# Optimization experiments

Hardware: AMD Instinct MI355X
Metric: run time of the kernel (lower is better)

The kernel has to match this reference:

```python
import jax, jax.numpy as jnp
import numpy as np
from jax import lax

H, W, C = 24, 8, 128
HW = H * W
PART = 4
SA_K = 49  # CBAM spatial-attention kernel size (default of CBAMBlock)
EPS = 1e-5


def conv2d(x, w, b, pad_h, pad_w):
    y = lax.conv_general_dilated(x, w, (1, 1), [(pad_h, pad_h), (pad_w, pad_w)],
                                 dimension_numbers=('NCHW', 'OIHW', 'NCHW'))
    return y + b[None, :, None, None]


def cbam(x, se_w1, se_w2, sa_w, sa_b):
    # Channel attention: shared MLP on global max- and avg-pooled descriptors.
    mx = x.max(axis=(2, 3))          # [n, c]
    av = x.mean(axis=(2, 3))         # [n, c]
    def se(v):
        return jax.nn.relu(v @ se_w1.T) @ se_w2.T
    ca = jax.nn.sigmoid(se(mx) + se(av))[:, :, None, None]
    out = x * ca
    # Spatial attention: 49x49 conv on [max, mean] over channels.
    smx = out.max(axis=1, keepdims=True)
    sav = out.mean(axis=1, keepdims=True)
    s = jnp.concatenate([smx, sav], axis=1)      # [n, 2, H, W]
    sa = jax.nn.sigmoid(conv2d(s, sa_w, sa_b, SA_K // 2, SA_K // 2))
    return out * sa + x


def position_aware_max(score6, dim):
    # score6: [p, g, hr, wr, hs, ws]; fixed-length (part_rows) row window,
    # start clamped to [0, h - part_rows] -> vectorized sliding-window max.
    part_rows = H // PART
    half = part_rows // 2
    starts = jnp.clip(jnp.arange(H) - half, 0, H - part_rows)
    if dim == 0:
        m = score6.max(axis=3)            # max over wr -> [p, g, hr, hs, ws]
        mi = jnp.moveaxis(m, 3, 0)        # [hs, p, g, hr, ws]
        def f(m_i, st):
            return lax.dynamic_slice_in_dim(m_i, st, part_rows, axis=2).max(axis=2)
        out = jax.vmap(f)(mi, starts)     # [h, p, g, ws]
    else:
        m = score6.max(axis=5)            # max over ws -> [p, g, hr, wr, hs]
        mi = jnp.moveaxis(m, 2, 0)        # [hr, p, g, wr, hs]
        def f(m_i, st):
            return lax.dynamic_slice_in_dim(m_i, st, part_rows, axis=3).max(axis=3)
        out = jax.vmap(f)(mi, starts)     # [h, p, g, wr]
    p, g = score6.shape[0], score6.shape[1]
    return jnp.moveaxis(out, 0, 2).reshape(p, g, HW)


def bn_eval(x, gamma, beta, mean, var):
    return (x - mean) * (gamma / jnp.sqrt(var + EPS)) + beta


def setup_inputs() -> dict:
    key = jax.random.key(0)
    ks = jax.random.split(key, 8)
    red = 16
    return {
        'prob_fea': jax.random.normal(ks[0], (32, C, H, W), jnp.float32),
        'gal_fea': jax.random.normal(ks[1], (32, C, H, W), jnp.float32),
        'se_w1': jax.random.normal(ks[2], (C // red, C), jnp.float32) * 0.05,
        'se_w2': jax.random.normal(ks[3], (C, C // red), jnp.float32) * 0.05,
        'sa_w': jax.random.normal(ks[4], (1, 2, SA_K, SA_K), jnp.float32) * 0.02,
        'sa_b': jnp.zeros((1,), jnp.float32),
        'bn_g': jnp.ones((1,), jnp.float32),
        'bn_b': jnp.zeros((1,), jnp.float32),
        'bn_m': jnp.zeros((1,), jnp.float32),
        'bn_v': jnp.ones((1,), jnp.float32),
        'fc_w': jnp.full((1, HW), 1.0 / HW, jnp.float32),
        'fc_b': jax.random.normal(ks[5], (1,), jnp.float32) * 0.01,
        'lbn_g': jnp.ones((1,), jnp.float32),
        'lbn_b': jnp.zeros((1,), jnp.float32),
        'lbn_m': jnp.zeros((1,), jnp.float32),
        'lbn_v': jnp.ones((1,), jnp.float32),
    }


def reference(prob_fea, gal_fea, se_w1, se_w2, sa_w, sa_b,
              bn_g, bn_b, bn_m, bn_v, fc_w, fc_b,
              lbn_g, lbn_b, lbn_m, lbn_v):
    pf = cbam(prob_fea, se_w1, se_w2, sa_w, sa_b)
    gf = cbam(gal_fea, se_w1, se_w2, sa_w, sa_b)
    p, g = pf.shape[0], gf.shape[0]
    pf = pf.reshape(p, C, HW)
    gf = gf.reshape(g, C, HW)
    # pairwise feature matching: [p, g, r(gal spatial), s(prob spatial)]
    score = jnp.einsum('pcs,gcr->pgrs', pf, gf)
    score6 = score.reshape(p, g, H, W, H, W)
    s1 = position_aware_max(score6, 0)  # [p, g, HW]
    s2 = position_aware_max(score6, 1)  # [p, g, HW]
    sc = jnp.concatenate([s1, s2], axis=-1).reshape(-1, HW)  # [p*g*2, HW]
    sc = bn_eval(sc, bn_g, bn_b, bn_m, bn_v)
    y = sc @ fc_w.T + fc_b                  # [p*g*2, 1]
    y = y.reshape(-1, 2).sum(axis=1, keepdims=True)
    y = bn_eval(y, lbn_g, lbn_b, lbn_m, lbn_v)
    return jax.nn.sigmoid(y).reshape(p, g)
```

## Files before the change

kernel.cpp:

```cpp
#include <hip/hip_runtime.h>
#include <hip/hip_bf16.h>

#define HH 24
#define WW 8
#define HWSZ 192
#define CC 128
#define EPSV 1e-5f

typedef __attribute__((ext_vector_type(8))) short bf16x8;
typedef __attribute__((ext_vector_type(4))) float f32x4;

__device__ __forceinline__ float sigmoidf_(float x) { return 1.0f / (1.0f + expf(-x)); }

__device__ __forceinline__ unsigned short f2bf(float f) {
    unsigned int u = __float_as_uint(f);
    unsigned int r = (u + 0x7fffu + ((u >> 16) & 1u)) >> 16;
    return (unsigned short)r;
}

__global__ __launch_bounds__(256) void cbam_kernel(
    const float* __restrict__ prob, const float* __restrict__ gal,
    const float* __restrict__ se_w1, const float* __restrict__ se_w2,
    const float* __restrict__ sa_w, const float* __restrict__ sa_b,
    __hip_bfloat16* __restrict__ pf_t, __hip_bfloat16* __restrict__ gf_t)
{
    __shared__ float mxs[CC], avs[CC], hid[16], cas[CC];
    __shared__ float smx[HWSZ], sav[HWSZ], sas[HWSZ];
    __shared__ float wbuf[2 * 49 * 49];

    int n = blockIdx.x;
    const float* x = (n < 32) ? prob + (size_t)n * CC * HWSZ : gal + (size_t)(n - 32) * CC * HWSZ;
    __hip_bfloat16* dst = (n < 32) ? pf_t + (size_t)n * HWSZ * CC : gf_t + (size_t)(n - 32) * HWSZ * CC;

    int tid = threadIdx.x, l = tid & 63, w = tid >> 6;

    for (int i = tid; i < 2 * 49 * 49; i += 256) wbuf[i] = sa_w[i];

    for (int c = w * 32; c < w * 32 + 32; ++c) {
        const float* row = x + c * HWSZ;
        float a = row[l], b = row[l + 64], d = row[l + 128];
        float mv = fmaxf(a, fmaxf(b, d));
        float sv = a + b + d;
        #pragma unroll
        for (int m = 1; m < 64; m <<= 1) {
            mv = fmaxf(mv, __shfl_xor(mv, m));
            sv += __shfl_xor(sv, m);
        }
        if (l == 0) { mxs[c] = mv; avs[c] = sv * (1.0f / HWSZ); }
    }
    __syncthreads();

    if (tid < 16) {
        int j = tid & 7;
        const float* v = (tid < 8) ? mxs : avs;
        float acc = 0.f;
        for (int c = 0; c < CC; ++c) acc += v[c] * se_w1[j * CC + c];
        hid[tid] = fmaxf(acc, 0.f);
    }
    __syncthreads();

    if (tid < CC) {
        float acc = 0.f;
        #pragma unroll
        for (int j = 0; j < 8; ++j) acc += (hid[j] + hid[8 + j]) * se_w2[tid * 8 + j];
        cas[tid] = sigmoidf_(acc);
    }
    __syncthreads();

    if (tid < HWSZ) {
        float mv = -INFINITY, sv = 0.f;
        for (int c = 0; c < CC; ++c) {
            float v = x[c * HWSZ + tid] * cas[c];
            mv = fmaxf(mv, v); sv += v;
        }
        smx[tid] = mv; sav[tid] = sv * (1.0f / CC);
    }
    __syncthreads();

    if (tid < HWSZ) {
        int y = tid >> 3, xx = tid & 7;
        float acc = sa_b[0];
        for (int iy = 0; iy < HH; ++iy) {
            int wy = iy - y + 24;
            const float* w0 = wbuf + wy * 49;
            const float* w1 = wbuf + 2401 + wy * 49;
            #pragma unroll
            for (int ix = 0; ix < WW; ++ix) {
                int wx = ix - xx + 24;
                float s0 = smx[iy * 8 + ix], s1 = sav[iy * 8 + ix];
                acc += s0 * w0[wx] + s1 * w1[wx];
            }
        }
        sas[tid] = sigmoidf_(acc);
    }
    __syncthreads();

    if (tid < HWSZ) {
        int s = tid;
        float sv = sas[s];
        unsigned int* dst32 = (unsigned int*)(dst + s * CC);
        for (int c = 0; c < CC; c += 2) {
            float v0 = x[c * HWSZ + s] * (1.f + cas[c] * sv);
            float v1 = x[(c + 1) * HWSZ + s] * (1.f + cas[c + 1] * sv);
            unsigned int pk = ((unsigned int)f2bf(v1) << 16) | (unsigned int)f2bf(v0);
            dst32[c >> 1] = pk;
        }
    }
}

__global__ __launch_bounds__(256) void score_kernel(
    const __hip_bfloat16* __restrict__ pf_t, const __hip_bfloat16* __restrict__ gf_t,
    const float* __restrict__ bn_g, const float* __restrict__ bn_b,
    const float* __restrict__ bn_m, const float* __restrict__ bn_v,
    const float* __restrict__ fc_w, const float* __restrict__ fc_b,
    const float* __restrict__ lbn_g, const float* __restrict__ lbn_b,
    const float* __restrict__ lbn_m, const float* __restrict__ lbn_v,
    float* __restrict__ out)
{
    __shared__ float M1[24 * HWSZ];
    __shared__ float M2[HWSZ * 24];
    __shared__ float red[8];

    int bi = blockIdx.x;
    int p = bi >> 5, g = bi & 31;
    int tid = threadIdx.x, l = tid & 63, w = tid >> 6;

    const __hip_bfloat16* A = gf_t + (size_t)g * HWSZ * CC;
    const __hip_bfloat16* B = pf_t + (size_t)p * HWSZ * CC;

    int row_a = l & 15;
    int koff = (l >> 4) * 8;

    bf16x8 afr[3][4];
    #pragma unroll
    for (int rt = 0; rt < 3; ++rt) {
        const __hip_bfloat16* ap = A + (w * 48 + rt * 16 + row_a) * CC + koff;
        #pragma unroll
        for (int ks = 0; ks < 4; ++ks)
            afr[rt][ks] = *(const bf16x8*)(ap + ks * 32);
    }

    for (int st = 0; st < 12; ++st) {
        bf16x8 bfr[4];
        const __hip_bfloat16* bp = B + (st * 16 + row_a) * CC + koff;
        #pragma unroll
        for (int ks = 0; ks < 4; ++ks) bfr[ks] = *(const bf16x8*)(bp + ks * 32);

        #pragma unroll
        for (int rt = 0; rt < 3; ++rt) {
            f32x4 acc = {0.f, 0.f, 0.f, 0.f};
            #pragma unroll
            for (int ks = 0; ks < 4; ++ks)
                acc = __builtin_amdgcn_mfma_f32_16x16x32_bf16(afr[rt][ks], bfr[ks], acc, 0, 0, 0);

            int RT = w * 3 + rt;

            float mrow = fmaxf(fmaxf(acc[0], acc[1]), fmaxf(acc[2], acc[3]));
            mrow = fmaxf(mrow, __shfl_xor(mrow, 16));
            if (((l >> 4) & 1) == 0)
                M1[(2 * RT + (l >> 5)) * HWSZ + st * 16 + (l & 15)] = mrow;

            float v0 = acc[0], v1 = acc[1], v2 = acc[2], v3 = acc[3];
            #pragma unroll
            for (int m = 1; m < 8; m <<= 1) {
                v0 = fmaxf(v0, __shfl_xor(v0, m));
                v1 = fmaxf(v1, __shfl_xor(v1, m));
                v2 = fmaxf(v2, __shfl_xor(v2, m));
                v3 = fmaxf(v3, __shfl_xor(v3, m));
            }
            if ((l & 7) == 0) {
                int hs = st * 2 + ((l >> 3) & 1);
                int rbase = RT * 16 + (l >> 4) * 4;
                M2[(rbase + 0) * 24 + hs] = v0;
                M2[(rbase + 1) * 24 + hs] = v1;
                M2[(rbase + 2) * 24 + hs] = v2;
                M2[(rbase + 3) * 24 + hs] = v3;
            }
        }
    }
    __syncthreads();

    float part = 0.f, wpart = 0.f;
    if (tid < HWSZ) {
        int h = tid >> 3;
        int st0 = h - 3; if (st0 < 0) st0 = 0; if (st0 > 18) st0 = 18;
        float v1 = -INFINITY, v2 = -INFINITY;
        #pragma unroll
        for (int i = 0; i < 6; ++i) {
            v1 = fmaxf(v1, M1[(st0 + i) * HWSZ + tid]);
            v2 = fmaxf(v2, M2[tid * 24 + st0 + i]);
        }
        float fw = fc_w[tid];
        part = fw * (v1 + v2);
        wpart = fw;
    }
    #pragma unroll
    for (int m = 1; m < 64; m <<= 1) {
        part  += __shfl_xor(part, m);
        wpart += __shfl_xor(wpart, m);
    }
    if (l == 0) { red[w] = part; red[4 + w] = wpart; }
    __syncthreads();

    if (tid == 0) {
        float total = red[0] + red[1] + red[2] + red[3];
        float Wsum  = red[4] + red[5] + red[6] + red[7];
        float k1 = bn_g[0] * rsqrtf(bn_v[0] + EPSV);
        float Y = k1 * total + 2.f * ((bn_b[0] - k1 * bn_m[0]) * Wsum + fc_b[0]);
        float kl = lbn_g[0] * rsqrtf(lbn_v[0] + EPSV);
        float Z = (Y - lbn_m[0]) * kl + lbn_b[0];
        out[bi] = 1.f / (1.f + expf(-Z));
    }
}

extern "C" void kernel_launch(void* const* d_in, const int* in_sizes, int n_in,
                              void* d_out, int out_size, void* d_ws, size_t ws_size,
                              hipStream_t stream)
{
    const float* prob  = (const float*)d_in[0];
    const float* gal   = (const float*)d_in[1];
    const float* se_w1 = (const float*)d_in[2];
    const float* se_w2 = (const float*)d_in[3];
    const float* sa_w  = (const float*)d_in[4];
    const float* sa_b  = (const float*)d_in[5];
    const float* bn_g  = (const float*)d_in[6];
    const float* bn_b  = (const float*)d_in[7];
    const float* bn_m  = (const float*)d_in[8];
    const float* bn_v  = (const float*)d_in[9];
    const float* fc_w  = (const float*)d_in[10];
    const float* fc_b  = (const float*)d_in[11];
    const float* lbn_g = (const float*)d_in[12];
    const float* lbn_b = (const float*)d_in[13];
    const float* lbn_m = (const float*)d_in[14];
    const float* lbn_v = (const float*)d_in[15];

    __hip_bfloat16* pf_t = (__hip_bfloat16*)d_ws;
    __hip_bfloat16* gf_t = pf_t + (size_t)32 * HWSZ * CC;
    float* out = (float*)d_out;

    cbam_kernel<<<64, 256, 0, stream>>>(prob, gal, se_w1, se_w2, sa_w, sa_b, pf_t, gf_t);
    score_kernel<<<1024, 256, 0, stream>>>(pf_t, gf_t, bn_g, bn_b, bn_m, bn_v,
                                           fc_w, fc_b, lbn_g, lbn_b, lbn_m, lbn_v, out);
}
```

Measured before the change: 157.9 us.

## Widen both kernels, store score maxima as bf16 in padded LDS, prefetch B

The CBAM kernel moves to 512 threads. It splits the channel reductions and the output write across two halves per spatial position, and it parallelises the first SE layer with shuffle reductions. The score kernel moves to 384 threads (6 waves, 2 row tiles each) and register-prefetches the next B fragment to overlap loads with MFMA. Its intermediate max maps are stored as bf16 in padded LDS to cut shared memory and bank conflicts. The bf16 storage of maxima adds rounding error before the windowed max and the FC reduction.

```diff
diff --git a/kernel.cpp b/kernel.cpp
--- a/kernel.cpp
+++ b/kernel.cpp
@@ -7,6 +7,9 @@
 #define CC 128
 #define EPSV 1e-5f
 
+#define M1LD 200
+#define M2LD 28
+
 typedef __attribute__((ext_vector_type(8))) short bf16x8;
 typedef __attribute__((ext_vector_type(4))) float f32x4;
 
@@ -17,15 +20,18 @@
     unsigned int r = (u + 0x7fffu + ((u >> 16) & 1u)) >> 16;
     return (unsigned short)r;
 }
-
-__global__ __launch_bounds__(256) void cbam_kernel(
+__device__ __forceinline__ float bf2f(unsigned short s) {
+    return __uint_as_float((unsigned int)s << 16);
+}
+
+__global__ __launch_bounds__(512) void cbam_kernel(
     const float* __restrict__ prob, const float* __restrict__ gal,
     const float* __restrict__ se_w1, const float* __restrict__ se_w2,
     const float* __restrict__ sa_w, const float* __restrict__ sa_b,
     __hip_bfloat16* __restrict__ pf_t, __hip_bfloat16* __restrict__ gf_t)
 {
     __shared__ float mxs[CC], avs[CC], hid[16], cas[CC];
-    __shared__ float smx[HWSZ], sav[HWSZ], sas[HWSZ];
+    __shared__ float smx2[2 * HWSZ], sav2[2 * HWSZ], sas[HWSZ];
     __shared__ float wbuf[2 * 49 * 49];
 
     int n = blockIdx.x;
@@ -34,9 +40,10 @@
 
     int tid = threadIdx.x, l = tid & 63, w = tid >> 6;
 
-    for (int i = tid; i < 2 * 49 * 49; i += 256) wbuf[i] = sa_w[i];
-
-    for (int c = w * 32; c < w * 32 + 32; ++c) {
+    for (int i = tid; i < 2 * 49 * 49; i += 512) wbuf[i] = sa_w[i];
+
+    for (int i = 0; i < 16; ++i) {
+        int c = w * 16 + i;
         const float* row = x + c * HWSZ;
         float a = row[l], b = row[l + 64], d = row[l + 128];
         float mv = fmaxf(a, fmaxf(b, d));
@@ -50,12 +57,17 @@
     }
     __syncthreads();
 
-    if (tid < 16) {
-        int j = tid & 7;
-        const float* v = (tid < 8) ? mxs : avs;
+    if (tid < 256) {
+        int j = tid >> 4, chunk = tid & 15;
+        const float* v = (j < 8) ? mxs : avs;
+        const float* wrow = se_w1 + (j & 7) * CC + chunk * 8;
+        const float* vv = v + chunk * 8;
         float acc = 0.f;
-        for (int c = 0; c < CC; ++c) acc += v[c] * se_w1[j * CC + c];
-        hid[tid] = fmaxf(acc, 0.f);
+        #pragma unroll
+        for (int k = 0; k < 8; ++k) acc += vv[k] * wrow[k];
+        #pragma unroll
+        for (int m = 1; m < 16; m <<= 1) acc += __shfl_xor(acc, m);
+        if (chunk == 0) hid[j] = fmaxf(acc, 0.f);
     }
     __syncthreads();
 
@@ -67,13 +79,16 @@
     }
     __syncthreads();
 
-    if (tid < HWSZ) {
+    if (tid < 2 * HWSZ) {
+        int s = tid >> 1, half = tid & 1;
+        int c0 = half * 64;
         float mv = -INFINITY, sv = 0.f;
-        for (int c = 0; c < CC; ++c) {
-            float v = x[c * HWSZ + tid] * cas[c];
+        #pragma unroll 4
+        for (int k = 0; k < 64; ++k) {
+            float v = x[(c0 + k) * HWSZ + s] * cas[c0 + k];
             mv = fmaxf(mv, v); sv += v;
         }
-        smx[tid] = mv; sav[tid] = sv * (1.0f / CC);
+        smx2[half * HWSZ + s] = mv; sav2[half * HWSZ + s] = sv;
     }
     __syncthreads();
 
@@ -87,7 +102,9 @@
             #pragma unroll
             for (int ix = 0; ix < WW; ++ix) {
                 int wx = ix - xx + 24;
-                float s0 = smx[iy * 8 + ix], s1 = sav[iy * 8 + ix];
+                int sp = iy * 8 + ix;
+                float s0 = fmaxf(smx2[sp], smx2[HWSZ + sp]);
+                float s1 = (sav2[sp] + sav2[HWSZ + sp]) * (1.0f / CC);
                 acc += s0 * w0[wx] + s1 * w1[wx];
             }
         }
@@ -95,20 +112,22 @@
     }
     __syncthreads();
 
-    if (tid < HWSZ) {
-        int s = tid;
+    if (tid < 2 * HWSZ) {
+        int s = tid >> 1, half = tid & 1;
+        int c0 = half * 64;
         float sv = sas[s];
-        unsigned int* dst32 = (unsigned int*)(dst + s * CC);
-        for (int c = 0; c < CC; c += 2) {
+        unsigned int* dst32 = (unsigned int*)(dst + s * CC) + half * 32;
+        #pragma unroll 4
+        for (int k = 0; k < 32; ++k) {
+            int c = c0 + 2 * k;
             float v0 = x[c * HWSZ + s] * (1.f + cas[c] * sv);
             float v1 = x[(c + 1) * HWSZ + s] * (1.f + cas[c + 1] * sv);
-            unsigned int pk = ((unsigned int)f2bf(v1) << 16) | (unsigned int)f2bf(v0);
-            dst32[c >> 1] = pk;
-        }
-    }
-}
-
-__global__ __launch_bounds__(256) void score_kernel(
+            dst32[k] = ((unsigned int)f2bf(v1) << 16) | (unsigned int)f2bf(v0);
+        }
+    }
+}
+
+__global__ __launch_bounds__(384) void score_kernel(
     const __hip_bfloat16* __restrict__ pf_t, const __hip_bfloat16* __restrict__ gf_t,
     const float* __restrict__ bn_g, const float* __restrict__ bn_b,
     const float* __restrict__ bn_m, const float* __restrict__ bn_v,
@@ -117,9 +136,9 @@
     const float* __restrict__ lbn_m, const float* __restrict__ lbn_v,
     float* __restrict__ out)
 {
-    __shared__ float M1[24 * HWSZ];
-    __shared__ float M2[HWSZ * 24];
-    __shared__ float red[8];
+    __shared__ unsigned short M1b[24 * M1LD];
+    __shared__ unsigned short M2b[HWSZ * M2LD];
+    __shared__ float red[6], wred[6];
 
     int bi = blockIdx.x;
     int p = bi >> 5, g = bi & 31;
@@ -131,34 +150,48 @@
     int row_a = l & 15;
     int koff = (l >> 4) * 8;
 
-    bf16x8 afr[3][4];
+    bf16x8 afr[2][4];
     #pragma unroll
-    for (int rt = 0; rt < 3; ++rt) {
-        const __hip_bfloat16* ap = A + (w * 48 + rt * 16 + row_a) * CC + koff;
+    for (int rt = 0; rt < 2; ++rt) {
+        const __hip_bfloat16* ap = A + (w * 32 + rt * 16 + row_a) * CC + koff;
         #pragma unroll
         for (int ks = 0; ks < 4; ++ks)
             afr[rt][ks] = *(const bf16x8*)(ap + ks * 32);
     }
 
+    bf16x8 b0, b1, b2, b3;
+    {
+        const __hip_bfloat16* bp = B + row_a * CC + koff;
+        b0 = *(const bf16x8*)(bp);
+        b1 = *(const bf16x8*)(bp + 32);
+        b2 = *(const bf16x8*)(bp + 64);
+        b3 = *(const bf16x8*)(bp + 96);
+    }
+
     for (int st = 0; st < 12; ++st) {
-        bf16x8 bfr[4];
-        const __hip_bfloat16* bp = B + (st * 16 + row_a) * CC + koff;
-        #pragma unroll
-        for (int ks = 0; ks < 4; ++ks) bfr[ks] = *(const bf16x8*)(bp + ks * 32);
-
-        #pragma unroll
-        for (int rt = 0; rt < 3; ++rt) {
+        bf16x8 n0, n1, n2, n3;
+        if (st < 11) {
+            const __hip_bfloat16* bp = B + ((st + 1) * 16 + row_a) * CC + koff;
+            n0 = *(const bf16x8*)(bp);
+            n1 = *(const bf16x8*)(bp + 32);
+            n2 = *(const bf16x8*)(bp + 64);
+            n3 = *(const bf16x8*)(bp + 96);
+        }
+
+        #pragma unroll
+        for (int rt = 0; rt < 2; ++rt) {
             f32x4 acc = {0.f, 0.f, 0.f, 0.f};
-            #pragma unroll
-            for (int ks = 0; ks < 4; ++ks)
-                acc = __builtin_amdgcn_mfma_f32_16x16x32_bf16(afr[rt][ks], bfr[ks], acc, 0, 0, 0);
-
-            int RT = w * 3 + rt;
+            acc = __builtin_amdgcn_mfma_f32_16x16x32_bf16(afr[rt][0], b0, acc, 0, 0, 0);
+            acc = __builtin_amdgcn_mfma_f32_16x16x32_bf16(afr[rt][1], b1, acc, 0, 0, 0);
+            acc = __builtin_amdgcn_mfma_f32_16x16x32_bf16(afr[rt][2], b2, acc, 0, 0, 0);
+            acc = __builtin_amdgcn_mfma_f32_16x16x32_bf16(afr[rt][3], b3, acc, 0, 0, 0);
+
+            int RT = w * 2 + rt;
 
             float mrow = fmaxf(fmaxf(acc[0], acc[1]), fmaxf(acc[2], acc[3]));
             mrow = fmaxf(mrow, __shfl_xor(mrow, 16));
             if (((l >> 4) & 1) == 0)
-                M1[(2 * RT + (l >> 5)) * HWSZ + st * 16 + (l & 15)] = mrow;
+                M1b[(2 * RT + (l >> 5)) * M1LD + st * 16 + (l & 15)] = f2bf(mrow);
 
             float v0 = acc[0], v1 = acc[1], v2 = acc[2], v3 = acc[3];
             #pragma unroll
@@ -171,12 +204,13 @@
             if ((l & 7) == 0) {
                 int hs = st * 2 + ((l >> 3) & 1);
                 int rbase = RT * 16 + (l >> 4) * 4;
-                M2[(rbase + 0) * 24 + hs] = v0;
-                M2[(rbase + 1) * 24 + hs] = v1;
-                M2[(rbase + 2) * 24 + hs] = v2;
-                M2[(rbase + 3) * 24 + hs] = v3;
+                M2b[(rbase + 0) * M2LD + hs] = f2bf(v0);
+                M2b[(rbase + 1) * M2LD + hs] = f2bf(v1);
+                M2b[(rbase + 2) * M2LD + hs] = f2bf(v2);
+                M2b[(rbase + 3) * M2LD + hs] = f2bf(v3);
             }
         }
+        b0 = n0; b1 = n1; b2 = n2; b3 = n3;
     }
     __syncthreads();
 
@@ -187,8 +221,8 @@
         float v1 = -INFINITY, v2 = -INFINITY;
         #pragma unroll
         for (int i = 0; i < 6; ++i) {
-            v1 = fmaxf(v1, M1[(st0 + i) * HWSZ + tid]);
-            v2 = fmaxf(v2, M2[tid * 24 + st0 + i]);
+            v1 = fmaxf(v1, bf2f(M1b[(st0 + i) * M1LD + tid]));
+            v2 = fmaxf(v2, bf2f(M2b[tid * M2LD + st0 + i]));
         }
         float fw = fc_w[tid];
         part = fw * (v1 + v2);
@@ -199,12 +233,12 @@
         part  += __shfl_xor(part, m);
         wpart += __shfl_xor(wpart, m);
     }
-    if (l == 0) { red[w] = part; red[4 + w] = wpart; }
+    if (l == 0) { red[w] = part; wred[w] = wpart; }
     __syncthreads();
 
     if (tid == 0) {
-        float total = red[0] + red[1] + red[2] + red[3];
-        float Wsum  = red[4] + red[5] + red[6] + red[7];
+        float total = red[0] + red[1] + red[2] + red[3] + red[4] + red[5];
+        float Wsum  = wred[0] + wred[1] + wred[2] + wred[3] + wred[4] + wred[5];
         float k1 = bn_g[0] * rsqrtf(bn_v[0] + EPSV);
         float Y = k1 * total + 2.f * ((bn_b[0] - k1 * bn_m[0]) * Wsum + fc_b[0]);
         float kl = lbn_g[0] * rsqrtf(lbn_v[0] + EPSV);
@@ -238,7 +272,7 @@
     __hip_bfloat16* gf_t = pf_t + (size_t)32 * HWSZ * CC;
     float* out = (float*)d_out;
 
-    cbam_kernel<<<64, 256, 0, stream>>>(prob, gal, se_w1, se_w2, sa_w, sa_b, pf_t, gf_t);
-    score_kernel<<<1024, 256, 0, stream>>>(pf_t, gf_t, bn_g, bn_b, bn_m, bn_v,
+    cbam_kernel<<<64, 512, 0, stream>>>(prob, gal, se_w1, se_w2, sa_w, sa_b, pf_t, gf_t);
+    score_kernel<<<1024, 384, 0, stream>>>(pf_t, gf_t, bn_g, bn_b, bn_m, bn_v,
                                            fc_w, fc_b, lbn_g, lbn_b, lbn_m, lbn_v, out);
 }
```

Measured after the change: 153.6 us. 2.7% less time.
